# Optimization experiments

Hardware: AMD Instinct MI355X
Metric: run time of the kernel (lower is better)

The kernel has to match this reference:

```python
import jax, jax.numpy as jnp
import numpy as np

N, D = 8192, 1024
TEMPERATURE = 0.1
EPS = 1e-8

def setup_inputs() -> dict:
    key = jax.random.key(0)
    k1, k2 = jax.random.split(key)
    emb = jax.random.normal(k1, (N, D), dtype=jnp.float32)
    # docstring: embeddings are normalized
    emb = emb / jnp.linalg.norm(emb, axis=1, keepdims=True)
    labels = jax.random.randint(k2, (N,), 0, 2, dtype=jnp.int32)
    return {"embeddings": emb, "labels": labels}

def reference(embeddings, labels):
    lab = labels.astype(embeddings.dtype)            # (N,)
    sim = jnp.matmul(embeddings, embeddings.T) / TEMPERATURE  # (N, N)
    exp_sim = jnp.exp(sim)                           # original uses raw exp (no max-subtract)
    diag = jnp.diagonal(exp_sim)                     # self-similarity exp(1/T)
    # all_sim excludes self; pos_sim = other reference rows (labels==1, j != i)
    all_sum = exp_sim.sum(axis=1) - diag             # (N,)
    pos_sum = exp_sim @ lab - diag * lab             # subtract self only when i is ref
    loss_per_row = -jnp.log(pos_sum / (all_sum + EPS))
    n_ref = lab.sum()
    loss = jnp.sum(jnp.where(lab > 0, loss_per_row, 0.0)) / jnp.maximum(n_ref, 1.0)
    # original returns 0.0 when fewer than 2 reference rows
    return jnp.where(n_ref < 2, jnp.array(0.0, embeddings.dtype), loss)
```

## Files before the change

kernel.cpp:

```cpp
#include <hip/hip_runtime.h>
#include <hip/hip_bf16.h>
#include <cstdint>
#include <cstddef>

#define NROWS 8192
#define DIM   1024
#define BM 128
#define BN 128
#define BK 64
#define NITER (DIM / BK)
#define EPS 1e-8f
#define PRESCALE 3.798283f

typedef short  bf16x8  __attribute__((ext_vector_type(8)));
typedef float  floatx4 __attribute__((ext_vector_type(4)));

__device__ __forceinline__ unsigned short f2bf_rne(float f) {
    union { float f; unsigned u; } c; c.f = f;
    unsigned u = c.u;
    unsigned r = (u + 0x7fffu + ((u >> 16) & 1u)) >> 16;
    return (unsigned short)r;
}

__global__ __launch_bounds__(256) void convert_kernel(
    const float* __restrict__ in, unsigned short* __restrict__ out,
    float* __restrict__ accum )
{
    int i = (blockIdx.x * 256 + threadIdx.x) * 4;
    float4 v = *(const float4*)(in + i);
    ushort4 o;
    o.x = f2bf_rne(v.x * PRESCALE);
    o.y = f2bf_rne(v.y * PRESCALE);
    o.z = f2bf_rne(v.z * PRESCALE);
    o.w = f2bf_rne(v.w * PRESCALE);
    *(ushort4*)(out + i) = o;
    if (blockIdx.x < (2 * NROWS) / 256)
        accum[blockIdx.x * 256 + threadIdx.x] = 0.0f;
}

__global__ __launch_bounds__(256, 3) void gemm_fused_kernel(
    const unsigned short* __restrict__ E,
    const int*            __restrict__ labels,
    float*                __restrict__ all_sum,
    float*                __restrict__ pos_sum)
{
    __shared__ __align__(16) unsigned short sA[BM * BK];
    __shared__ __align__(16) unsigned short sB[BN * BK];

    const int tid  = threadIdx.x;
    const int lane = tid & 63;
    const int w    = tid >> 6;
    const int wm   = w >> 1;
    const int wn   = w & 1;
    const int colw = lane & 15;
    const int quad = lane >> 4;

    const int t = blockIdx.x;
    int bi = (int)((sqrtf(8.0f * (float)t + 1.0f) - 1.0f) * 0.5f);
    while ((bi + 1) * (bi + 2) / 2 <= t) ++bi;
    while (bi * (bi + 1) / 2 > t) --bi;
    const int bj = t - bi * (bi + 1) / 2;

    const int rBase = bi * BM;
    const int cBase = bj * BN;
    const bool diag = (bi == bj);

    const int srow = tid >> 3;
    const int scol = (((tid & 7) ^ (srow & 7)) << 3);
    const int e0   = tid * 8;

    floatx4 acc[4][4];
    #pragma unroll
    for (int i = 0; i < 4; ++i)
        #pragma unroll
        for (int j = 0; j < 4; ++j)
            acc[i][j] = (floatx4)0.0f;

    const int swz   = colw & 7;
    const int aRow0 = (wm * 64 + colw) * BK;
    const int bRow0 = (wn * 64 + colw) * BK;

    const size_t gA0 = (size_t)(rBase + srow) * DIM + scol;
    const size_t gB0 = (size_t)(cBase + srow) * DIM + scol;
    const size_t rstep = (size_t)32 * DIM;

    bf16x8 rA[4], rB[4];

    #pragma unroll
    for (int j = 0; j < 4; ++j) {
        rA[j] = *(const bf16x8*)(E + gA0 + j * rstep);
        rB[j] = *(const bf16x8*)(E + gB0 + j * rstep);
    }

    #pragma unroll
    for (int it = 0; it < NITER; ++it) {
        #pragma unroll
        for (int j = 0; j < 4; ++j) {
            *(bf16x8*)&sA[e0 + j * 2048] = rA[j];
            *(bf16x8*)&sB[e0 + j * 2048] = rB[j];
        }
        if (it + 1 < NITER) {
            const size_t kOff = (size_t)(it + 1) * BK;
            #pragma unroll
            for (int j = 0; j < 4; ++j) {
                rA[j] = *(const bf16x8*)(E + gA0 + j * rstep + kOff);
                rB[j] = *(const bf16x8*)(E + gB0 + j * rstep + kOff);
            }
        }
        asm volatile("s_waitcnt lgkmcnt(0)\n\ts_barrier" ::: "memory");

        #pragma unroll
        for (int h = 0; h < 2; ++h) {
            const int cOff = (((h << 2) | quad) ^ swz) << 3;
            bf16x8 aF[4], bF[4];
            #pragma unroll
            for (int mt = 0; mt < 4; ++mt)
                aF[mt] = *(const bf16x8*)&sA[aRow0 + mt * 16 * BK + cOff];
            #pragma unroll
            for (int nt = 0; nt < 4; ++nt)
                bF[nt] = *(const bf16x8*)&sB[bRow0 + nt * 16 * BK + cOff];

            #pragma unroll
            for (int mt = 0; mt < 4; ++mt)
                #pragma unroll
                for (int nt = 0; nt < 4; ++nt)
                    acc[mt][nt] = __builtin_amdgcn_mfma_f32_16x16x32_bf16(
                        aF[mt], bF[nt], acc[mt][nt], 0, 0, 0);
        }
        if (it + 1 < NITER)
            asm volatile("s_barrier" ::: "memory");
    }

    float labc[4];
    int   gcol[4];
    #pragma unroll
    for (int nt = 0; nt < 4; ++nt) {
        gcol[nt] = cBase + wn * 64 + nt * 16 + colw;
        labc[nt] = (float)labels[gcol[nt]];
    }

    float colAll[4] = {0.f, 0.f, 0.f, 0.f};
    float colPos[4] = {0.f, 0.f, 0.f, 0.f};

    #pragma unroll
    for (int mt = 0; mt < 4; ++mt) {
        const int growBase = rBase + wm * 64 + mt * 16 + quad * 4;
        #pragma unroll
        for (int r = 0; r < 4; ++r) {
            const int grow = growBase + r;
            const float labr = (float)labels[grow];
            float sAll = 0.f, sPos = 0.f;
            #pragma unroll
            for (int nt = 0; nt < 4; ++nt) {
                float ev = exp2f(acc[mt][nt][r]);
                if (diag && grow == gcol[nt]) ev = 0.0f;
                sAll += ev;
                sPos += ev * labc[nt];
                colAll[nt] += ev;
                colPos[nt] += ev * labr;
            }
            #pragma unroll
            for (int off = 1; off < 16; off <<= 1) {
                sAll += __shfl_xor(sAll, off);
                sPos += __shfl_xor(sPos, off);
            }
            if (colw == 0) {
                atomicAdd(&all_sum[grow], sAll);
                atomicAdd(&pos_sum[grow], sPos);
            }
        }
    }

    if (!diag) {
        #pragma unroll
        for (int nt = 0; nt < 4; ++nt) {
            float a = colAll[nt], p = colPos[nt];
            a += __shfl_xor(a, 16);  p += __shfl_xor(p, 16);
            a += __shfl_xor(a, 32);  p += __shfl_xor(p, 32);
            if (quad == 0) {
                atomicAdd(&all_sum[gcol[nt]], a);
                atomicAdd(&pos_sum[gcol[nt]], p);
            }
        }
    }
}

__global__ __launch_bounds__(1024) void finalize_kernel(
    const float* __restrict__ all_sum,
    const float* __restrict__ pos_sum,
    const int*   __restrict__ labels,
    float*       __restrict__ out)
{
    __shared__ float sSum[1024];
    __shared__ float sCnt[1024];
    const int tid = threadIdx.x;
    float lsum = 0.f, lcnt = 0.f;
    for (int i = tid; i < NROWS; i += 1024) {
        if (labels[i] > 0) {
            float p = pos_sum[i];
            float a = all_sum[i] + EPS;
            lsum += -logf(p / a);
            lcnt += 1.0f;
        }
    }
    sSum[tid] = lsum;
    sCnt[tid] = lcnt;
    __syncthreads();
    for (int s = 512; s > 0; s >>= 1) {
        if (tid < s) { sSum[tid] += sSum[tid + s]; sCnt[tid] += sCnt[tid + s]; }
        __syncthreads();
    }
    if (tid == 0) {
        float n = sCnt[0];
        out[0] = (n < 2.0f) ? 0.0f : sSum[0] / fmaxf(n, 1.0f);
    }
}

extern "C" void kernel_launch(void* const* d_in, const int* in_sizes, int n_in,
                              void* d_out, int out_size, void* d_ws, size_t ws_size,
                              hipStream_t stream) {
    const float* emb    = (const float*)d_in[0];
    const int*   labels = (const int*)d_in[1];
    float*       out    = (float*)d_out;

    unsigned short* Ebf = (unsigned short*)d_ws;
    const size_t embBytes = (size_t)NROWS * DIM * sizeof(unsigned short);
    float* all_sum = (float*)((char*)d_ws + embBytes);
    float* pos_sum = all_sum + NROWS;

    convert_kernel<<<(NROWS * DIM) / (4 * 256), 256, 0, stream>>>(emb, Ebf, all_sum);

    const int nBlocksTri = (NROWS / BM) * (NROWS / BM + 1) / 2;
    gemm_fused_kernel<<<nBlocksTri, 256, 0, stream>>>(Ebf, labels, all_sum, pos_sum);

    finalize_kernel<<<1, 1024, 0, stream>>>(all_sum, pos_sum, labels, out);
}
```

Measured before the change: 213.9 us.

## Use direct global-to-LDS loads, XCD-aware tile order, and fuse finalize via ticket

Global-to-register-to-LDS staging is replaced with global_load_lds direct async loads, which frees registers so the launch bound can raise occupancy from 3 to 5 blocks per SIMD. Triangular tile indices are remapped so blocks with the same low 3 bits (same XCD) share column strips, aiming for better L2 reuse. The separate finalize kernel is removed: the last block, chosen by an atomic ticket, computes the loss. In exchange the loop now has two full barriers per K step and no register double-buffering, so load latency is exposed unless occupancy hides it.

```diff
diff --git a/kernel.cpp b/kernel.cpp
--- a/kernel.cpp
+++ b/kernel.cpp
@@ -9,11 +9,20 @@
 #define BN 128
 #define BK 64
 #define NITER (DIM / BK)
+#define NTILE (NROWS / BM)
+#define NBLK  2080
 #define EPS 1e-8f
-#define PRESCALE 3.798283f
+#define PRESCALE 3.798288f
 
 typedef short  bf16x8  __attribute__((ext_vector_type(8)));
 typedef float  floatx4 __attribute__((ext_vector_type(4)));
+
+typedef __attribute__((address_space(1))) const void CGV;
+typedef __attribute__((address_space(3))) void LV;
+
+__device__ __forceinline__ void async_load16(const void* g, void* l) {
+    __builtin_amdgcn_global_load_lds((CGV*)g, (LV*)l, 16, 0, 0);
+}
 
 __device__ __forceinline__ unsigned short f2bf_rne(float f) {
     union { float f; unsigned u; } c; c.f = f;
@@ -24,7 +33,7 @@
 
 __global__ __launch_bounds__(256) void convert_kernel(
     const float* __restrict__ in, unsigned short* __restrict__ out,
-    float* __restrict__ accum )
+    float* __restrict__ accum , int* __restrict__ ticket)
 {
     int i = (blockIdx.x * 256 + threadIdx.x) * 4;
     float4 v = *(const float4*)(in + i);
@@ -36,16 +45,21 @@
     *(ushort4*)(out + i) = o;
     if (blockIdx.x < (2 * NROWS) / 256)
         accum[blockIdx.x * 256 + threadIdx.x] = 0.0f;
-}
-
-__global__ __launch_bounds__(256, 3) void gemm_fused_kernel(
+    if (blockIdx.x == 64 && threadIdx.x == 0)
+        *ticket = 0;
+}
+
+__global__ __launch_bounds__(256, 5) void gemm_fused_kernel(
     const unsigned short* __restrict__ E,
     const int*            __restrict__ labels,
     float*                __restrict__ all_sum,
-    float*                __restrict__ pos_sum)
+    float*                __restrict__ pos_sum,
+    int*                  __restrict__ ticket,
+    float*                __restrict__ out)
 {
     __shared__ __align__(16) unsigned short sA[BM * BK];
     __shared__ __align__(16) unsigned short sB[BN * BK];
+    __shared__ int sTicket;
 
     const int tid  = threadIdx.x;
     const int lane = tid & 63;
@@ -55,11 +69,24 @@
     const int colw = lane & 15;
     const int quad = lane >> 4;
 
-    const int t = blockIdx.x;
-    int bi = (int)((sqrtf(8.0f * (float)t + 1.0f) - 1.0f) * 0.5f);
-    while ((bi + 1) * (bi + 2) / 2 <= t) ++bi;
-    while (bi * (bi + 1) / 2 > t) --bi;
-    const int bj = t - bi * (bi + 1) / 2;
+    const int b  = blockIdx.x;
+    const int x  = b & 7;
+    int       p  = b >> 3;
+    const int k0 = x << 2;
+    int bi = 0, bj = 0;
+    for (;;) {
+        int lo = (k0 + 4) - ((bj > k0) ? bj : k0);
+        lo = (lo < 0) ? 0 : ((lo > 4) ? 4 : lo);
+        int up = 64 - bj - k0;
+        up = (up < 0) ? 0 : ((up > 4) ? 4 : up);
+        const int c = lo + up;
+        if (p < c) {
+            if (p < lo) bi = ((bj > k0) ? bj : k0) + p;
+            else        bi = 63 - (k0 + (p - lo));
+            break;
+        }
+        p -= c; ++bj;
+    }
 
     const int rBase = bi * BM;
     const int cBase = bj * BN;
@@ -84,30 +111,17 @@
     const size_t gB0 = (size_t)(cBase + srow) * DIM + scol;
     const size_t rstep = (size_t)32 * DIM;
 
-    bf16x8 rA[4], rB[4];
-
-    #pragma unroll
-    for (int j = 0; j < 4; ++j) {
-        rA[j] = *(const bf16x8*)(E + gA0 + j * rstep);
-        rB[j] = *(const bf16x8*)(E + gB0 + j * rstep);
-    }
-
-    #pragma unroll
-    for (int it = 0; it < NITER; ++it) {
-        #pragma unroll
-        for (int j = 0; j < 4; ++j) {
-            *(bf16x8*)&sA[e0 + j * 2048] = rA[j];
-            *(bf16x8*)&sB[e0 + j * 2048] = rB[j];
-        }
-        if (it + 1 < NITER) {
-            const size_t kOff = (size_t)(it + 1) * BK;
-            #pragma unroll
-            for (int j = 0; j < 4; ++j) {
-                rA[j] = *(const bf16x8*)(E + gA0 + j * rstep + kOff);
-                rB[j] = *(const bf16x8*)(E + gB0 + j * rstep + kOff);
-            }
-        }
-        asm volatile("s_waitcnt lgkmcnt(0)\n\ts_barrier" ::: "memory");
+    for (int k0i = 0; k0i < DIM; k0i += BK) {
+        __syncthreads();
+        async_load16(E + gA0 + k0i,             &sA[e0]);
+        async_load16(E + gA0 + rstep + k0i,     &sA[e0 + 2048]);
+        async_load16(E + gA0 + 2 * rstep + k0i, &sA[e0 + 4096]);
+        async_load16(E + gA0 + 3 * rstep + k0i, &sA[e0 + 6144]);
+        async_load16(E + gB0 + k0i,             &sB[e0]);
+        async_load16(E + gB0 + rstep + k0i,     &sB[e0 + 2048]);
+        async_load16(E + gB0 + 2 * rstep + k0i, &sB[e0 + 4096]);
+        async_load16(E + gB0 + 3 * rstep + k0i, &sB[e0 + 6144]);
+        __syncthreads();
 
         #pragma unroll
         for (int h = 0; h < 2; ++h) {
@@ -127,8 +141,6 @@
                     acc[mt][nt] = __builtin_amdgcn_mfma_f32_16x16x32_bf16(
                         aF[mt], bF[nt], acc[mt][nt], 0, 0, 0);
         }
-        if (it + 1 < NITER)
-            asm volatile("s_barrier" ::: "memory");
     }
 
     float labc[4];
@@ -174,45 +186,42 @@
     if (!diag) {
         #pragma unroll
         for (int nt = 0; nt < 4; ++nt) {
-            float a = colAll[nt], p = colPos[nt];
-            a += __shfl_xor(a, 16);  p += __shfl_xor(p, 16);
-            a += __shfl_xor(a, 32);  p += __shfl_xor(p, 32);
+            float a = colAll[nt], pq = colPos[nt];
+            a += __shfl_xor(a, 16);  pq += __shfl_xor(pq, 16);
+            a += __shfl_xor(a, 32);  pq += __shfl_xor(pq, 32);
             if (quad == 0) {
                 atomicAdd(&all_sum[gcol[nt]], a);
-                atomicAdd(&pos_sum[gcol[nt]], p);
-            }
-        }
-    }
-}
-
-__global__ __launch_bounds__(1024) void finalize_kernel(
-    const float* __restrict__ all_sum,
-    const float* __restrict__ pos_sum,
-    const int*   __restrict__ labels,
-    float*       __restrict__ out)
-{
-    __shared__ float sSum[1024];
-    __shared__ float sCnt[1024];
-    const int tid = threadIdx.x;
-    float lsum = 0.f, lcnt = 0.f;
-    for (int i = tid; i < NROWS; i += 1024) {
-        if (labels[i] > 0) {
-            float p = pos_sum[i];
-            float a = all_sum[i] + EPS;
-            lsum += -logf(p / a);
-            lcnt += 1.0f;
-        }
-    }
-    sSum[tid] = lsum;
-    sCnt[tid] = lcnt;
+                atomicAdd(&pos_sum[gcol[nt]], pq);
+            }
+        }
+    }
+
+    __threadfence();
+    if (tid == 0) sTicket = atomicAdd(ticket, 1);
     __syncthreads();
-    for (int s = 512; s > 0; s >>= 1) {
-        if (tid < s) { sSum[tid] += sSum[tid + s]; sCnt[tid] += sCnt[tid + s]; }
+    if (sTicket == NBLK - 1) {
+        __threadfence();
+        float lsum = 0.f, lcnt = 0.f;
+        for (int i = tid; i < NROWS; i += 256) {
+            if (labels[i] > 0) {
+                lsum += -logf(pos_sum[i] / (all_sum[i] + EPS));
+                lcnt += 1.0f;
+            }
+        }
+        #pragma unroll
+        for (int off = 1; off < 64; off <<= 1) {
+            lsum += __shfl_xor(lsum, off);
+            lcnt += __shfl_xor(lcnt, off);
+        }
+        float* red = (float*)sA;
+        if (lane == 0) { red[w * 2] = lsum; red[w * 2 + 1] = lcnt; }
         __syncthreads();
-    }
-    if (tid == 0) {
-        float n = sCnt[0];
-        out[0] = (n < 2.0f) ? 0.0f : sSum[0] / fmaxf(n, 1.0f);
+        if (tid == 0) {
+            float S = 0.f, C = 0.f;
+            #pragma unroll
+            for (int j = 0; j < 4; ++j) { S += red[j * 2]; C += red[j * 2 + 1]; }
+            out[0] = (C < 2.0f) ? 0.0f : S / fmaxf(C, 1.0f);
+        }
     }
 }
 
@@ -227,11 +236,9 @@
     const size_t embBytes = (size_t)NROWS * DIM * sizeof(unsigned short);
     float* all_sum = (float*)((char*)d_ws + embBytes);
     float* pos_sum = all_sum + NROWS;
-
-    convert_kernel<<<(NROWS * DIM) / (4 * 256), 256, 0, stream>>>(emb, Ebf, all_sum);
-
-    const int nBlocksTri = (NROWS / BM) * (NROWS / BM + 1) / 2;
-    gemm_fused_kernel<<<nBlocksTri, 256, 0, stream>>>(Ebf, labels, all_sum, pos_sum);
-
-    finalize_kernel<<<1, 1024, 0, stream>>>(all_sum, pos_sum, labels, out);
-}
+    int*   ticket  = (int*)(pos_sum + NROWS);
+
+    convert_kernel<<<(NROWS * DIM) / (4 * 256), 256, 0, stream>>>(emb, Ebf, all_sum, ticket);
+
+    gemm_fused_kernel<<<NBLK, 256, 0, stream>>>(Ebf, labels, all_sum, pos_sum, ticket, out);
+}
```

Measured after the change: 325.5 us. +52.2%, slower.
